# Kernel tuning notes

Measured on AMD Instinct MI355X. Metric: run time of the kernel, lower is better.

Reference implementation:

```python
import jax, jax.numpy as jnp
import numpy as np

HH = 38  # sqrt(amd0=1444)
KD = 3   # 3x3 neighborhood


def setup_inputs() -> dict:
    key = jax.random.key(0)
    fm = jax.random.normal(key, (16, 512, HH, HH), dtype=jnp.float32)
    return {"fm": fm}


def reference(fm):
    # fm: [B, C, H, W] -> replication pad 1 -> NHWC -> gather 3x3 neighbors,
    # concatenated along the channel axis in row-major neighbor order
    # (matching counts[:, 0..8] = (h-1,w-1),(h-1,w),(h-1,w+1),(h,w-1),...).
    B, C, H, W = fm.shape
    x = jnp.pad(fm, ((0, 0), (0, 0), (1, 1), (1, 1)), mode="edge")  # [B,C,H+2,W+2]
    x = jnp.transpose(x, (0, 2, 3, 1))  # [B, H+2, W+2, C]
    patches = [x[:, di:di + H, dj:dj + W, :] for di in range(KD) for dj in range(KD)]
    pfm = jnp.concatenate(patches, axis=-1)  # [B, H, W, 9*C]
    return pfm.reshape(B, H * W, KD * KD * C)  # [B, 1444, 9*C]
```

## Files before the change

kernel.cpp:

```cpp
#include <hip/hip_runtime.h>


#define BB 16
#define CC 512
#define HH 38
#define WW 38
#define HW (HH * WW)
#define KK 9
#define NT 256
#define NW4 10

__global__ __launch_bounds__(NT) void spatial_pool_scatter(
    const float* __restrict__ fm, float* __restrict__ out)
{
    const int blk   = blockIdx.x;
    const int w4    = blk % NW4;
    const int t     = blk / NW4;
    const int chalf = t & 1;
    const int bh    = t >> 1;
    const int h     = bh % HH;
    const int b     = bh / HH;
    const int c     = chalf * NT + threadIdx.x;

    const int w0 = w4 * 4;
    const int nw = (w4 == NW4 - 1) ? 2 : 4;

    const float* src = fm + ((size_t)(b * CC + c)) * HW + h * WW + w0;
    float v[4];
    {
        float2 r0 = *(const float2*)src;
        v[0] = r0.x; v[1] = r0.y;
        if (nw == 4) {
            float2 r1 = *(const float2*)(src + 2);
            v[2] = r1.x; v[3] = r1.y;
        }
    }

    int hrow[3];
    {
        int n = 0;
        #pragma unroll
        for (int di = 0; di < 3; ++di) {
            int hm = h + 1 - di;
            if (0 <= hm && hm < HH) { hrow[n] = (b * HW + hm * WW) * KK + di * 3; n++; }
        }
        if (h == 0)      { hrow[n] = (b * HW) * KK; n++; }
        if (h == HH - 1) { hrow[n] = (b * HW + (HH - 1) * WW) * KK + 6; n++; }
    }

    for (int wi = 0; wi < nw; ++wi) {
        const int w = w0 + wi;
        int woff[3];
        {
            int m = 0;
            #pragma unroll
            for (int dj = 0; dj < 3; ++dj) {
                int wm = w + 1 - dj;
                if (0 <= wm && wm < WW) { woff[m] = wm * KK + dj; m++; }
            }
            if (w == 0)      { woff[m] = 0; m++; }
            if (w == WW - 1) { woff[m] = (WW - 1) * KK + 2; m++; }
        }
        const float val = v[wi];
        #pragma unroll
        for (int i = 0; i < 3; ++i) {
            #pragma unroll
            for (int j = 0; j < 3; ++j) {
                unsigned idx = (unsigned)(hrow[i] + woff[j]) * (unsigned)CC + (unsigned)c;
                __builtin_nontemporal_store(val, out + (size_t)idx);
            }
        }
    }
}

extern "C" void kernel_launch(void* const* d_in, const int* in_sizes, int n_in,
                              void* d_out, int out_size, void* d_ws, size_t ws_size,
                              hipStream_t stream) {
    const float* fm = (const float*)d_in[0];
    float* out = (float*)d_out;
    dim3 grid(NW4 * 2 * BB * HH);
    dim3 block(NT);
    spatial_pool_scatter<<<grid, block, 0, stream>>>(fm, out);
}
```

Before: 462.6 us.

## Process a full image row per block with all 512 channels per thread block

Each block now handles one (batch, row) pair with 512 threads covering every channel. Each thread loads its whole 38-wide row into registers and scatters all 9 neighbor copies for every column. This removes the split across width-quarters and channel halves, which cuts per-block index math and the number of small loads. In exchange the grid shrinks to 608 blocks, which may underfill the GPU. Each thread also holds 38 floats in registers, and per-thread loads along a row are strided by HW across channels, so reads are not coalesced.

```diff
diff --git a/kernel.cpp b/kernel.cpp
--- a/kernel.cpp
+++ b/kernel.cpp
@@ -7,33 +7,23 @@
 #define WW 38
 #define HW (HH * WW)
 #define KK 9
-#define NT 256
-#define NW4 10
+#define NT 512
 
 __global__ __launch_bounds__(NT) void spatial_pool_scatter(
     const float* __restrict__ fm, float* __restrict__ out)
 {
-    const int blk   = blockIdx.x;
-    const int w4    = blk % NW4;
-    const int t     = blk / NW4;
-    const int chalf = t & 1;
-    const int bh    = t >> 1;
-    const int h     = bh % HH;
-    const int b     = bh / HH;
-    const int c     = chalf * NT + threadIdx.x;
+    const int bh = blockIdx.x;
+    const int h  = bh % HH;
+    const int b  = bh / HH;
+    const int c  = threadIdx.x;
 
-    const int w0 = w4 * 4;
-    const int nw = (w4 == NW4 - 1) ? 2 : 4;
-
-    const float* src = fm + ((size_t)(b * CC + c)) * HW + h * WW + w0;
-    float v[4];
-    {
-        float2 r0 = *(const float2*)src;
-        v[0] = r0.x; v[1] = r0.y;
-        if (nw == 4) {
-            float2 r1 = *(const float2*)(src + 2);
-            v[2] = r1.x; v[3] = r1.y;
-        }
+    const float* src = fm + ((size_t)(b * CC + c)) * HW + h * WW;
+    float v[WW];
+    #pragma unroll
+    for (int i = 0; i < WW / 2; ++i) {
+        const float2 r = *((const float2*)src + i);
+        v[2 * i + 0] = r.x;
+        v[2 * i + 1] = r.y;
     }
 
     int hrow[3];
@@ -48,26 +38,25 @@
         if (h == HH - 1) { hrow[n] = (b * HW + (HH - 1) * WW) * KK + 6; n++; }
     }
 
-    for (int wi = 0; wi < nw; ++wi) {
-        const int w = w0 + wi;
+    float* outc = out + c;
+    #pragma unroll
+    for (int w = 0; w < WW; ++w) {
         int woff[3];
-        {
-            int m = 0;
-            #pragma unroll
-            for (int dj = 0; dj < 3; ++dj) {
-                int wm = w + 1 - dj;
-                if (0 <= wm && wm < WW) { woff[m] = wm * KK + dj; m++; }
-            }
-            if (w == 0)      { woff[m] = 0; m++; }
-            if (w == WW - 1) { woff[m] = (WW - 1) * KK + 2; m++; }
+        int m = 0;
+        #pragma unroll
+        for (int dj = 0; dj < 3; ++dj) {
+            int wm = w + 1 - dj;
+            if (0 <= wm && wm < WW) { woff[m] = wm * KK + dj; m++; }
         }
-        const float val = v[wi];
+        if (w == 0)      { woff[m] = 0; m++; }
+        if (w == WW - 1) { woff[m] = (WW - 1) * KK + 2; m++; }
+        const float val = v[w];
         #pragma unroll
         for (int i = 0; i < 3; ++i) {
             #pragma unroll
             for (int j = 0; j < 3; ++j) {
-                unsigned idx = (unsigned)(hrow[i] + woff[j]) * (unsigned)CC + (unsigned)c;
-                __builtin_nontemporal_store(val, out + (size_t)idx);
+                unsigned idx = (unsigned)(hrow[i] + woff[j]) * (unsigned)CC;
+                __builtin_nontemporal_store(val, outc + (size_t)idx);
             }
         }
     }
@@ -78,7 +67,7 @@
                               hipStream_t stream) {
     const float* fm = (const float*)d_in[0];
     float* out = (float*)d_out;
-    dim3 grid(NW4 * 2 * BB * HH);
+    dim3 grid(BB * HH);
     dim3 block(NT);
     spatial_pool_scatter<<<grid, block, 0, stream>>>(fm, out);
 }
```

Result: faster. 451.2 us (-2.5%).
